# Kernel optimization log

Hardware: AMD Instinct MI355X
Metric: run time of the kernel (lower is better)

Reference implementation:

```python
import jax, jax.numpy as jnp
import numpy as np

OUT_SIZE = 7          # RoIAlign output resolution
SPATIAL_SCALE = 1.0 / 16.0


def _make_boxes(n, im_sz, rng):
    # valid [x1,y1,x2,y2] boxes in image coordinates (0..im_sz)
    x1 = rng.uniform(0.0, im_sz * 0.7, size=n)
    y1 = rng.uniform(0.0, im_sz * 0.7, size=n)
    w = rng.uniform(16.0, im_sz * 0.5, size=n)
    h = rng.uniform(16.0, im_sz * 0.5, size=n)
    x2 = np.minimum(x1 + w, im_sz - 1.0)
    y2 = np.minimum(y1 + h, im_sz - 1.0)
    return np.stack([x1, y1, x2, y2], axis=1).astype(np.float32)


def setup_inputs() -> dict:
    key = jax.random.key(0)
    V, F, C, H, W = 8, 16, 1024, 14, 14
    N = 768
    features = jax.random.normal(key, (V, F, C, H, W), dtype=jnp.float32)
    rng = np.random.default_rng(0)
    boxes = jnp.asarray(_make_boxes(N, 224, rng))
    frame_idx = jnp.asarray(rng.integers(0, V * F, size=N), dtype=jnp.int32)
    return {"features": features, "boxes": boxes, "frame_idx": frame_idx}


def _roi_align_avg(features, boxes, frame_idx, out_size=OUT_SIZE, scale=SPATIAL_SCALE):
    """Legacy RoIAlignAvg: bilinear-sample an (out+1)x(out+1) grid spanning the
    scaled box, then 2x2 stride-1 average pool -> [N, C, out, out]."""
    V, F, C, H, W = features.shape
    flat = features.reshape(V * F, C, H, W).transpose(0, 2, 3, 1)  # [M, H, W, C]
    G = out_size + 1
    x1, y1, x2, y2 = (boxes[:, i] * scale for i in range(4))
    t = jnp.linspace(0.0, 1.0, G, dtype=boxes.dtype)               # [G]
    xs = jnp.clip(x1[:, None] + t[None, :] * (x2 - x1)[:, None], 0.0, W - 1)  # [N, G]
    ys = jnp.clip(y1[:, None] + t[None, :] * (y2 - y1)[:, None], 0.0, H - 1)  # [N, G]
    x0 = jnp.floor(xs).astype(jnp.int32); x1i = jnp.minimum(x0 + 1, W - 1)
    y0 = jnp.floor(ys).astype(jnp.int32); y1i = jnp.minimum(y0 + 1, H - 1)
    wx = (xs - x0)[:, None, :, None]   # [N, 1, G, 1]
    wy = (ys - y0)[:, :, None, None]   # [N, G, 1, 1]
    b = frame_idx[:, None, None]
    # gathers -> [N, G(y), G(x), C]
    g00 = flat[b, y0[:, :, None], x0[:, None, :]]
    g01 = flat[b, y0[:, :, None], x1i[:, None, :]]
    g10 = flat[b, y1i[:, :, None], x0[:, None, :]]
    g11 = flat[b, y1i[:, :, None], x1i[:, None, :]]
    val = ((1.0 - wy) * ((1.0 - wx) * g00 + wx * g01)
           + wy * ((1.0 - wx) * g10 + wx * g11))         # [N, G, G, C]
    pooled = 0.25 * (val[:, :-1, :-1] + val[:, 1:, :-1]
                     + val[:, :-1, 1:] + val[:, 1:, 1:])  # [N, out, out, C]
    return pooled.transpose(0, 3, 1, 2)                   # [N, C, out, out]


def reference(features, boxes, frame_idx):
    # Batched equivalent of the per-video/per-box Python loop:
    # 1) per-box RoIAlignAvg node features (H_Node / O_Node / H_O_Node path)
    roi_feats = _roi_align_avg(features, boxes, frame_idx)
    # 2) S_node: global spatial mean per frame feature map
    s_node = features.mean(axis=(-2, -1))          # [V, F, C]
    # 3) Fake_H_S: 12x12 center crop (S_node_pre[:, :, 1:13, 1:13])
    fake_h_s = features[..., 1:13, 1:13]           # [V, F, C, 12, 12]
    return roi_feats, s_node, fake_h_s
```

## Files before the change

kernel.cpp:

```cpp
#include <hip/hip_runtime.h>

constexpr int VF = 128;
constexpr int C  = 1024;
constexpr int H  = 14;
constexpr int W  = 14;
constexpr int HW = H * W;
constexpr int NBOX = 768;
constexpr int OUTSZ = 7;
constexpr float SCALE = 1.0f / 16.0f;

constexpr long long ROI_ELEMS  = (long long)NBOX * C * OUTSZ * OUTSZ;
constexpr long long SNODE_ELEMS = (long long)VF * C;

__global__ void roi_kernel(const float* __restrict__ feat,
                           const float* __restrict__ boxes,
                           const int* __restrict__ fidx,
                           float* __restrict__ out) {
    const int lane  = threadIdx.x & 63;
    const int wave  = (blockIdx.x * blockDim.x + threadIdx.x) >> 6;
    const int nwav  = (gridDim.x * blockDim.x) >> 6;
    const int total = NBOX * C;

    const int gy = lane >> 3;
    const int gx = lane & 7;
    const float tx = (float)gx * (1.0f / 7.0f);
    const float ty = (float)gy * (1.0f / 7.0f);

    for (int task = wave; task < total; task += nwav) {
        const int n = task >> 10;
        const int c = task & 1023;

        const float bx1 = boxes[n * 4 + 0] * SCALE;
        const float by1 = boxes[n * 4 + 1] * SCALE;
        const float bx2 = boxes[n * 4 + 2] * SCALE;
        const float by2 = boxes[n * 4 + 3] * SCALE;
        const int b = fidx[n];

        const float* f = feat + ((size_t)b * C + c) * HW;

        float xs = bx1 + tx * (bx2 - bx1);
        float ys = by1 + ty * (by2 - by1);
        xs = fminf(fmaxf(xs, 0.0f), (float)(W - 1));
        ys = fminf(fmaxf(ys, 0.0f), (float)(H - 1));

        const int x0 = (int)floorf(xs);
        const int y0 = (int)floorf(ys);
        const int x1 = min(x0 + 1, W - 1);
        const int y1 = min(y0 + 1, H - 1);
        const float wx = xs - (float)x0;
        const float wy = ys - (float)y0;

        const float f00 = f[y0 * W + x0];
        const float f01 = f[y0 * W + x1];
        const float f10 = f[y1 * W + x0];
        const float f11 = f[y1 * W + x1];

        const float top = f00 + wx * (f01 - f00);
        const float bot = f10 + wx * (f11 - f10);
        const float val = top + wy * (bot - top);

        const float v_r  = __shfl(val, lane + 1, 64);
        const float v_d  = __shfl(val, lane + 8, 64);
        const float v_dr = __shfl(val, lane + 9, 64);

        if (gy < OUTSZ && gx < OUTSZ) {
            const float p = 0.25f * (val + v_r + v_d + v_dr);
            out[(((size_t)n * C + c) * OUTSZ + gy) * OUTSZ + gx] = p;
        }
    }
}

__global__ void tail_kernel(const float* __restrict__ feat,
                            float* __restrict__ s_node,
                            float* __restrict__ fake) {
    const int lane  = threadIdx.x & 63;
    const int wave  = (blockIdx.x * blockDim.x + threadIdx.x) >> 6;
    const int nwav  = (gridDim.x * blockDim.x) >> 6;
    const int total = VF * C;

    for (int task = wave; task < total; task += nwav) {
        const float* f = feat + (size_t)task * HW;

        float s = f[lane] + f[lane + 64] + f[lane + 128];
        if (lane < 4) s += f[lane + 192];
        #pragma unroll
        for (int off = 32; off; off >>= 1) s += __shfl_down(s, off, 64);
        if (lane == 0) s_node[task] = s * (1.0f / 196.0f);

        float* o = fake + (size_t)task * 144;
        {
            int oi = lane;
            int yy = oi / 12, xx = oi - yy * 12;
            o[oi] = f[(yy + 1) * W + xx + 1];
        }
        {
            int oi = lane + 64;
            int yy = oi / 12, xx = oi - yy * 12;
            o[oi] = f[(yy + 1) * W + xx + 1];
        }
        if (lane < 16) {
            int oi = lane + 128;
            int yy = oi / 12, xx = oi - yy * 12;
            o[oi] = f[(yy + 1) * W + xx + 1];
        }
    }
}

extern "C" void kernel_launch(void* const* d_in, const int* in_sizes, int n_in,
                              void* d_out, int out_size, void* d_ws, size_t ws_size,
                              hipStream_t stream) {
    const float* feat  = (const float*)d_in[0];
    const float* boxes = (const float*)d_in[1];
    const int*   fidx  = (const int*)d_in[2];

    float* roi    = (float*)d_out;
    float* s_node = roi + ROI_ELEMS;
    float* fake   = s_node + SNODE_ELEMS;

    roi_kernel<<<2048, 256, 0, stream>>>(feat, boxes, fidx, roi);
    tail_kernel<<<2048, 256, 0, stream>>>(feat, s_node, fake);
}
```

Before: 431.7 us.

## Fuse RoI and tail kernels, chunk channels per wave, vectorize tail loads

Merges the RoIAlign and the mean/crop kernels into one launch, with separate wave ranges handling each part so they run concurrently. Each RoI wave now processes a 64-channel chunk of one box, computing the box geometry and bilinear weights once and looping over channels with unrolling. The tail path uses float4 loads for the mean and float4 stores for the crop, with gather indices precomputed once per wave. The aim is to cut redundant per-task box setup, launch overhead, and narrow memory transactions. In exchange the work split between the two parts is fixed statically, which may leave the load unbalanced.

```diff
diff --git a/kernel.cpp b/kernel.cpp
--- a/kernel.cpp
+++ b/kernel.cpp
@@ -9,99 +9,105 @@
 constexpr int OUTSZ = 7;
 constexpr float SCALE = 1.0f / 16.0f;
 
-constexpr long long ROI_ELEMS  = (long long)NBOX * C * OUTSZ * OUTSZ;
+constexpr long long ROI_ELEMS   = (long long)NBOX * C * OUTSZ * OUTSZ;
 constexpr long long SNODE_ELEMS = (long long)VF * C;
 
-__global__ void roi_kernel(const float* __restrict__ feat,
-                           const float* __restrict__ boxes,
-                           const int* __restrict__ fidx,
-                           float* __restrict__ out) {
-    const int lane  = threadIdx.x & 63;
-    const int wave  = (blockIdx.x * blockDim.x + threadIdx.x) >> 6;
-    const int nwav  = (gridDim.x * blockDim.x) >> 6;
-    const int total = NBOX * C;
+constexpr int ROI_CHUNKS   = 16;
+constexpr int CH_PER_CHUNK = C / ROI_CHUNKS;
+constexpr int ROI_WAVES    = NBOX * ROI_CHUNKS;
+constexpr int TAIL_WAVES   = 4096;
+constexpr int TOTAL_WAVES  = ROI_WAVES + TAIL_WAVES;
+constexpr int TAIL_TASKS   = VF * C;
 
-    const int gy = lane >> 3;
-    const int gx = lane & 7;
-    const float tx = (float)gx * (1.0f / 7.0f);
-    const float ty = (float)gy * (1.0f / 7.0f);
+__global__ __launch_bounds__(256) void fused_kernel(
+    const float* __restrict__ feat,
+    const float* __restrict__ boxes,
+    const int*   __restrict__ fidx,
+    float* __restrict__ roi,
+    float* __restrict__ s_node,
+    float* __restrict__ fake)
+{
+    const int lane = threadIdx.x & 63;
+    const int w    = (blockIdx.x * blockDim.x + threadIdx.x) >> 6;
 
-    for (int task = wave; task < total; task += nwav) {
-        const int n = task >> 10;
-        const int c = task & 1023;
+    if (w < ROI_WAVES) {
+        const int n     = w >> 4;
+        const int chunk = w & 15;
 
         const float bx1 = boxes[n * 4 + 0] * SCALE;
         const float by1 = boxes[n * 4 + 1] * SCALE;
         const float bx2 = boxes[n * 4 + 2] * SCALE;
         const float by2 = boxes[n * 4 + 3] * SCALE;
-        const int b = fidx[n];
+        const int   b   = fidx[n];
 
-        const float* f = feat + ((size_t)b * C + c) * HW;
+        const int gy = lane >> 3;
+        const int gx = lane & 7;
 
-        float xs = bx1 + tx * (bx2 - bx1);
-        float ys = by1 + ty * (by2 - by1);
+        float xs = bx1 + ((float)gx * (1.0f / 7.0f)) * (bx2 - bx1);
+        float ys = by1 + ((float)gy * (1.0f / 7.0f)) * (by2 - by1);
         xs = fminf(fmaxf(xs, 0.0f), (float)(W - 1));
         ys = fminf(fmaxf(ys, 0.0f), (float)(H - 1));
-
         const int x0 = (int)floorf(xs);
         const int y0 = (int)floorf(ys);
         const int x1 = min(x0 + 1, W - 1);
         const int y1 = min(y0 + 1, H - 1);
         const float wx = xs - (float)x0;
         const float wy = ys - (float)y0;
+        const float w11 = wx * wy;
+        const float w10 = wy - w11;
+        const float w01 = wx - w11;
+        const float w00 = 1.0f - wx - wy + w11;
+        const int o00 = y0 * W + x0;
+        const int o01 = y0 * W + x1;
+        const int o10 = y1 * W + x0;
+        const int o11 = y1 * W + x1;
 
-        const float f00 = f[y0 * W + x0];
-        const float f01 = f[y0 * W + x1];
-        const float f10 = f[y1 * W + x0];
-        const float f11 = f[y1 * W + x1];
+        const float* f  = feat + ((size_t)b * C + (size_t)chunk * CH_PER_CHUNK) * HW;
+        float*       op = roi + ((size_t)n * C + (size_t)chunk * CH_PER_CHUNK) * (OUTSZ * OUTSZ)
+                              + (gy * OUTSZ + gx);
+        const bool active = (gy < OUTSZ) && (gx < OUTSZ);
 
-        const float top = f00 + wx * (f01 - f00);
-        const float bot = f10 + wx * (f11 - f10);
-        const float val = top + wy * (bot - top);
+        #pragma unroll 4
+        for (int cc = 0; cc < CH_PER_CHUNK; ++cc) {
+            const float* fc = f + cc * HW;
+            const float v = w00 * fc[o00] + w01 * fc[o01]
+                          + w10 * fc[o10] + w11 * fc[o11];
+            const float vr  = __shfl(v, lane + 1, 64);
+            const float vd  = __shfl(v, lane + 8, 64);
+            const float vdr = __shfl(v, lane + 9, 64);
+            if (active) op[cc * (OUTSZ * OUTSZ)] = 0.25f * (v + vr + vd + vdr);
+        }
+    } else {
+        const int tw = w - ROI_WAVES;
 
-        const float v_r  = __shfl(val, lane + 1, 64);
-        const float v_d  = __shfl(val, lane + 8, 64);
-        const float v_dr = __shfl(val, lane + 9, 64);
+        int i0 = 0, i1 = 0, i2 = 0, i3 = 0;
+        if (lane < 36) {
+            const int o = lane * 4;
+            i0 = ((o    ) / 12 + 1) * W + (o    ) % 12 + 1;
+            i1 = ((o + 1) / 12 + 1) * W + (o + 1) % 12 + 1;
+            i2 = ((o + 2) / 12 + 1) * W + (o + 2) % 12 + 1;
+            i3 = ((o + 3) / 12 + 1) * W + (o + 3) % 12 + 1;
+        }
 
-        if (gy < OUTSZ && gx < OUTSZ) {
-            const float p = 0.25f * (val + v_r + v_d + v_dr);
-            out[(((size_t)n * C + c) * OUTSZ + gy) * OUTSZ + gx] = p;
-        }
-    }
-}
+        for (int task = tw; task < TAIL_TASKS; task += TAIL_WAVES) {
+            const float* f = feat + (size_t)task * HW;
 
-__global__ void tail_kernel(const float* __restrict__ feat,
-                            float* __restrict__ s_node,
-                            float* __restrict__ fake) {
-    const int lane  = threadIdx.x & 63;
-    const int wave  = (blockIdx.x * blockDim.x + threadIdx.x) >> 6;
-    const int nwav  = (gridDim.x * blockDim.x) >> 6;
-    const int total = VF * C;
+            float4 v;
+            if (lane < 49) v = ((const float4*)f)[lane];
+            else           v = make_float4(0.f, 0.f, 0.f, 0.f);
+            float s = v.x + v.y + v.z + v.w;
+            #pragma unroll
+            for (int off = 32; off; off >>= 1) s += __shfl_down(s, off, 64);
+            if (lane == 0) s_node[task] = s * (1.0f / 196.0f);
 
-    for (int task = wave; task < total; task += nwav) {
-        const float* f = feat + (size_t)task * HW;
-
-        float s = f[lane] + f[lane + 64] + f[lane + 128];
-        if (lane < 4) s += f[lane + 192];
-        #pragma unroll
-        for (int off = 32; off; off >>= 1) s += __shfl_down(s, off, 64);
-        if (lane == 0) s_node[task] = s * (1.0f / 196.0f);
-
-        float* o = fake + (size_t)task * 144;
-        {
-            int oi = lane;
-            int yy = oi / 12, xx = oi - yy * 12;
-            o[oi] = f[(yy + 1) * W + xx + 1];
-        }
-        {
-            int oi = lane + 64;
-            int yy = oi / 12, xx = oi - yy * 12;
-            o[oi] = f[(yy + 1) * W + xx + 1];
-        }
-        if (lane < 16) {
-            int oi = lane + 128;
-            int yy = oi / 12, xx = oi - yy * 12;
-            o[oi] = f[(yy + 1) * W + xx + 1];
+            if (lane < 36) {
+                float4 o4;
+                o4.x = f[i0];
+                o4.y = f[i1];
+                o4.z = f[i2];
+                o4.w = f[i3];
+                ((float4*)(fake + (size_t)task * 144))[lane] = o4;
+            }
         }
     }
 }
@@ -117,6 +123,6 @@
     float* s_node = roi + ROI_ELEMS;
     float* fake   = s_node + SNODE_ELEMS;
 
-    roi_kernel<<<2048, 256, 0, stream>>>(feat, boxes, fidx, roi);
-    tail_kernel<<<2048, 256, 0, stream>>>(feat, s_node, fake);
+    fused_kernel<<<TOTAL_WAVES / 4, 256, 0, stream>>>(feat, boxes, fidx,
+                                                      roi, s_node, fake);
 }
```

Measured after the change: 366.1 us. -15.2%, faster.
